# Kernel tuning notes

Measured on AMD Instinct MI355X. Metric: run time of the kernel, lower is better.

The kernel has to match this reference:

```python
import jax, jax.numpy as jnp
import numpy as np

HEADS = 20
SHIFT = 0.6931471805599453  # style_alignment_score_shift = log(2)
KEY_SCALE = 1.0             # style_alignment_score_scale
EPS = 1e-5


def expand_first(feat, scale=1.0):
    # feat: [B, H, S, D]; broadcast style features (batch items 0 and B//2)
    b = feat.shape[0]
    fs = jnp.stack([feat[0], feat[b // 2]])[:, None]           # [2,1,H,S,D]
    fs = jnp.broadcast_to(fs, (2, b // 2) + feat.shape[1:])    # [2,B/2,H,S,D]
    if scale != 1:
        fs = jnp.concatenate([fs[:, :1], scale * fs[:, 1:]], axis=1)
    return fs.reshape(feat.shape)


def concat_first(feat, scale=1.0):
    # concatenate style features along the sequence axis (-2)
    return jnp.concatenate([feat, expand_first(feat, scale=scale)], axis=-2)


def adain(feat):
    # stats over sequence axis (-2); torch .var() is unbiased (ddof=1)
    mean = feat.mean(axis=-2, keepdims=True)
    std = jnp.sqrt(feat.var(axis=-2, keepdims=True, ddof=1) + EPS)
    sm = expand_first(mean)
    ss = expand_first(std)
    return (feat - mean) / std * ss + sm


def setup_inputs() -> dict:
    key = jax.random.key(0)
    ks = jax.random.split(key, 6)
    B, S, C = 4, 1024, 1280
    sc = 1.0 / np.sqrt(C)
    return {
        "hidden_states": jax.random.normal(ks[0], (B, S, C), jnp.float32),
        "Wq": jax.random.normal(ks[1], (C, C), jnp.float32) * sc,
        "Wk": jax.random.normal(ks[2], (C, C), jnp.float32) * sc,
        "Wv": jax.random.normal(ks[3], (C, C), jnp.float32) * sc,
        "Wo": jax.random.normal(ks[4], (C, C), jnp.float32) * sc,
        "bo": jnp.zeros((C,), jnp.float32),
    }


def reference(hidden_states, Wq, Wk, Wv, Wo, bo):
    B, S, C = hidden_states.shape
    H = HEADS
    hd = C // H
    scale = hd ** -0.5

    def to_heads(t):  # [B,S,C] -> [B,H,S,hd]
        return t.reshape(B, S, H, hd).transpose(0, 2, 1, 3)

    q = to_heads(hidden_states @ Wq.T)
    k = to_heads(hidden_states @ Wk.T)
    v = to_heads(hidden_states @ Wv.T)

    q = adain(q)              # adain_queries
    k = adain(k)              # adain_keys
    # adain_values = False

    k = concat_first(k, scale=KEY_SCALE)   # [B,H,2S,hd]
    v = concat_first(v)                    # [B,H,2S,hd]

    # shifted scaled dot-product attention (shift added to shared-key block)
    logits = jnp.einsum('bhqd,bhkd->bhqk', q, k) * scale  # [B,H,S,2S]
    bias = jnp.where(jnp.arange(k.shape[-2]) >= S, jnp.float32(SHIFT), jnp.float32(0.0))
    probs = jax.nn.softmax(logits + bias, axis=-1)
    out = jnp.einsum('bhqk,bhkd->bhqd', probs, v)         # [B,H,S,hd]

    out = out.transpose(0, 2, 1, 3).reshape(B, S, C)
    out = out @ Wo.T + bo
    return out
```

## Files before the change

kernel.cpp:

```cpp
#include <hip/hip_runtime.h>
#include <math.h>


typedef __bf16 bf16x8 __attribute__((ext_vector_type(8)));
typedef __bf16 bf16x2_t __attribute__((ext_vector_type(2)));
typedef float f32x4 __attribute__((ext_vector_type(4)));
typedef unsigned short u16x8 __attribute__((ext_vector_type(8)));

#define BDIM 256

__device__ inline unsigned short f2bf(float f) {
  return __builtin_bit_cast(unsigned short, (__bf16)f);
}
__device__ inline unsigned int pack_bf2(float lo, float hi) {
  bf16x2_t v;
  v[0] = (__bf16)lo;
  v[1] = (__bf16)hi;
  return __builtin_bit_cast(unsigned int, v);
}
__device__ inline float bf2f(unsigned short h) {
  return __uint_as_float(((unsigned int)h) << 16);
}

__device__ inline void gl_lds16(const unsigned short* g, unsigned short* l) {
  __builtin_amdgcn_global_load_lds(
      (const __attribute__((address_space(1))) unsigned int*)g,
      (__attribute__((address_space(3))) unsigned int*)l, 16, 0, 0);
}

__global__ __launch_bounds__(BDIM) void k_convert_all(
    const float* __restrict__ X, const float* __restrict__ Wq,
    const float* __restrict__ Wk, const float* __restrict__ Wv,
    const float* __restrict__ Wo, unsigned short* __restrict__ Xbf,
    unsigned short* __restrict__ Wcat, unsigned short* __restrict__ Wobf) {
  const int idx = blockIdx.x * BDIM + threadIdx.x;
  const float* src;
  unsigned short* dst;
  int off;
  if (idx < 1310720) {
    src = X; dst = Xbf; off = idx;
  } else {
    const int r = idx - 1310720;
    const int which = r / 409600;
    off = r - which * 409600;
    src = (which == 0) ? Wq : (which == 1) ? Wk : (which == 2) ? Wv : Wo;
    dst = (which < 3) ? Wcat + (size_t)which * 1638400 : Wobf;
  }
  const float4 v = ((const float4*)src)[off];
  ushort4 o;
  o.x = f2bf(v.x); o.y = f2bf(v.y); o.z = f2bf(v.z); o.w = f2bf(v.w);
  ((ushort4*)dst)[off] = o;
}

__global__ __launch_bounds__(512, 1) void k_gemm_bf16(
    const unsigned short* __restrict__ A, const unsigned short* __restrict__ B,
    unsigned short* __restrict__ qb, unsigned short* __restrict__ kb,
    unsigned short* __restrict__ vb, int M, int N, int K) {
  __shared__ unsigned short lds[4][2][256 * 32];

  const int bid = blockIdx.x;
  const int swz = (bid & 7) * 30 + (bid >> 3);
  const int mt = swz & 15, nt = swz >> 4;
  const int mBase = mt * 256, nBase = nt * 256;
  const int r3 = nt / 5;
  unsigned short* Cb = (r3 == 0) ? qb : (r3 == 1) ? kb : vb;
  const int nOff = nBase - r3 * 1280;

  const int t = threadIdx.x;
  const int w = t >> 6, lane = t & 63, quad = lane >> 4, l16 = lane & 15;
  const int wrow = w & 1, wcol = w >> 1;
  const int NTILES = K >> 5;

  f32x4 acc[8][4];
#pragma unroll
  for (int i = 0; i < 8; ++i)
#pragma unroll
    for (int j = 0; j < 4; ++j) acc[i][j] = (f32x4){0.f, 0.f, 0.f, 0.f};

  const int srow = t >> 2;
  const int sgl = ((t & 3) ^ ((t >> 3) & 3)) * 8;

  auto stage = [&](int s, int kt) {
#pragma unroll
    for (int j = 0; j < 2; ++j) {
      const int row = j * 128 + srow;
      gl_lds16(A + (size_t)(mBase + row) * K + kt * 32 + sgl,
               &lds[s][0][(j * 512 + t) * 8]);
    }
#pragma unroll
    for (int j = 0; j < 2; ++j) {
      const int row = j * 128 + srow;
      gl_lds16(B + (size_t)(nBase + row) * K + kt * 32 + sgl,
               &lds[s][1][(j * 512 + t) * 8]);
    }
  };

  stage(0, 0);
  stage(1, 1);

  const int arow0 = (wrow * 128 + l16) * 32;
  const int brow0 = (wcol * 64 + l16) * 32;
  const int gsw = (quad ^ ((l16 >> 1) & 3)) * 8;

  for (int kt = 0; kt < NTILES; ++kt) {
    const int s = kt & 3;
    if (kt + 2 < NTILES) {
      stage((kt + 2) & 3, kt + 2);
      asm volatile("s_waitcnt vmcnt(8)" ::: "memory");
    } else if (kt + 1 < NTILES) {
      asm volatile("s_waitcnt vmcnt(4)" ::: "memory");
    } else {
      asm volatile("s_waitcnt vmcnt(0)" ::: "memory");
    }
    __builtin_amdgcn_s_barrier();

    const unsigned short* As = &lds[s][0][0];
    const unsigned short* Bs = &lds[s][1][0];
    bf16x8 af[8], bq[4];
#pragma unroll
    for (int mi = 0; mi < 8; ++mi)
      af[mi] = *(const bf16x8*)(As + arow0 + mi * 512 + gsw);
#pragma unroll
    for (int ni = 0; ni < 4; ++ni)
      bq[ni] = *(const bf16x8*)(Bs + brow0 + ni * 512 + gsw);
    __builtin_amdgcn_s_setprio(1);
#pragma unroll
    for (int mi = 0; mi < 8; ++mi)
#pragma unroll
      for (int ni = 0; ni < 4; ++ni)
        acc[mi][ni] = __builtin_amdgcn_mfma_f32_16x16x32_bf16(
            af[mi], bq[ni], acc[mi][ni], 0, 0, 0);
    __builtin_amdgcn_s_setprio(0);
  }

#pragma unroll
  for (int mi = 0; mi < 8; ++mi)
#pragma unroll
    for (int r = 0; r < 4; ++r) {
      const int row = mBase + wrow * 128 + mi * 16 + quad * 4 + r;
#pragma unroll
      for (int ni = 0; ni < 4; ++ni)
        Cb[(size_t)row * 1280 + nOff + wcol * 64 + ni * 16 + l16] =
            f2bf(acc[mi][ni][r]);
    }
}

__global__ __launch_bounds__(BDIM, 2) void k_gemm_out(
    const unsigned short* __restrict__ A, const unsigned short* __restrict__ B,
    float* __restrict__ Cf, const float* __restrict__ bias, int M, int N,
    int K) {
  __shared__ unsigned short lds[4][2][128 * 32];

  const int bid = blockIdx.x;
  const int swz = (bid & 7) * 40 + (bid >> 3);
  const int mt = swz & 31, nt = swz >> 5;
  const int mBase = mt * 128, nBase = nt * 128;

  const int t = threadIdx.x;
  const int w = t >> 6, lane = t & 63, quad = lane >> 4, l16 = lane & 15;
  const int wrow = w & 1, wcol = w >> 1;
  const int NTILES = K >> 5;

  f32x4 acc[4][4];
#pragma unroll
  for (int i = 0; i < 4; ++i)
#pragma unroll
    for (int j = 0; j < 4; ++j) acc[i][j] = (f32x4){0.f, 0.f, 0.f, 0.f};

  const int srow = t >> 2;
  const int sgl = ((t & 3) ^ ((t >> 3) & 3)) * 8;

  auto stage = [&](int s, int kt) {
#pragma unroll
    for (int j = 0; j < 2; ++j) {
      const int row = j * 64 + srow;
      gl_lds16(A + (size_t)(mBase + row) * K + kt * 32 + sgl,
               &lds[s][0][(j * 256 + t) * 8]);
    }
#pragma unroll
    for (int j = 0; j < 2; ++j) {
      const int row = j * 64 + srow;
      gl_lds16(B + (size_t)(nBase + row) * K + kt * 32 + sgl,
               &lds[s][1][(j * 256 + t) * 8]);
    }
  };

  stage(0, 0);
  stage(1, 1);

  const int arow0 = (wrow * 64 + l16) * 32;
  const int brow0 = (wcol * 64 + l16) * 32;
  const int gsw = (quad ^ ((l16 >> 1) & 3)) * 8;

  for (int kt = 0; kt < NTILES; ++kt) {
    const int s = kt & 3;
    if (kt + 2 < NTILES) {
      stage((kt + 2) & 3, kt + 2);
      asm volatile("s_waitcnt vmcnt(8)" ::: "memory");
    } else if (kt + 1 < NTILES) {
      asm volatile("s_waitcnt vmcnt(4)" ::: "memory");
    } else {
      asm volatile("s_waitcnt vmcnt(0)" ::: "memory");
    }
    __builtin_amdgcn_s_barrier();

    const unsigned short* As = &lds[s][0][0];
    const unsigned short* Bs = &lds[s][1][0];
    bf16x8 af[4], bq[4];
#pragma unroll
    for (int mi = 0; mi < 4; ++mi)
      af[mi] = *(const bf16x8*)(As + arow0 + mi * 512 + gsw);
#pragma unroll
    for (int ni = 0; ni < 4; ++ni)
      bq[ni] = *(const bf16x8*)(Bs + brow0 + ni * 512 + gsw);
    __builtin_amdgcn_s_setprio(1);
#pragma unroll
    for (int mi = 0; mi < 4; ++mi)
#pragma unroll
      for (int ni = 0; ni < 4; ++ni)
        acc[mi][ni] = __builtin_amdgcn_mfma_f32_16x16x32_bf16(
            af[mi], bq[ni], acc[mi][ni], 0, 0, 0);
    __builtin_amdgcn_s_setprio(0);
  }

#pragma unroll
  for (int mi = 0; mi < 4; ++mi)
#pragma unroll
    for (int r = 0; r < 4; ++r) {
      const int row = mBase + wrow * 64 + mi * 16 + quad * 4 + r;
#pragma unroll
      for (int ni = 0; ni < 4; ++ni) {
        const int col = nBase + wcol * 64 + ni * 16 + l16;
        Cf[(size_t)row * N + col] = acc[mi][ni][r] + bias[col];
      }
    }
}

__global__ __launch_bounds__(320) void k_stats1(
    const unsigned short* __restrict__ qb, const unsigned short* __restrict__ kb,
    float* __restrict__ psum, float* __restrict__ psq) {
  const int z = blockIdx.y, which = z >> 2, b = z & 3;
  const unsigned short* src = (which == 0) ? qb : kb;
  const int c = threadIdx.x * 4;
  const size_t base = (size_t)(b * 1024 + blockIdx.x * 32) * 1280 + c;
  float4 s = {0.f, 0.f, 0.f, 0.f}, s2 = {0.f, 0.f, 0.f, 0.f};
#pragma unroll 8
  for (int i = 0; i < 32; ++i) {
    const ushort4 xv = *(const ushort4*)(src + base + (size_t)i * 1280);
    const float x0 = bf2f(xv.x), x1 = bf2f(xv.y), x2 = bf2f(xv.z),
                x3 = bf2f(xv.w);
    s.x += x0; s.y += x1; s.z += x2; s.w += x3;
    s2.x = fmaf(x0, x0, s2.x); s2.y = fmaf(x1, x1, s2.y);
    s2.z = fmaf(x2, x2, s2.z); s2.w = fmaf(x3, x3, s2.w);
  }
  const size_t o = ((size_t)z * 32 + blockIdx.x) * 1280 + c;
  *(float4*)(psum + o) = s;
  *(float4*)(psq + o) = s2;
}

__global__ __launch_bounds__(BDIM) void k_vt_stats2(
    const unsigned short* __restrict__ vb, unsigned short* __restrict__ vt,
    const float* __restrict__ psum, const float* __restrict__ psq,
    float* __restrict__ fst) {
  const int bx = blockIdx.x;
  if (bx >= 1280) {
    const int fb = bx - 1280;
    const int which = fb / 5;
    const int c = (fb % 5) * 256 + threadIdx.x;
    float m[4], sd[4];
#pragma unroll
    for (int b = 0; b < 4; ++b) {
      const int z = which * 4 + b;
      float s = 0.f, s2 = 0.f;
#pragma unroll
      for (int j = 0; j < 32; ++j) {
        s += psum[((size_t)z * 32 + j) * 1280 + c];
        s2 += psq[((size_t)z * 32 + j) * 1280 + c];
      }
      const float mean = s * (1.0f / 1024.0f);
      const float var = (s2 - 1024.0f * mean * mean) * (1.0f / 1023.0f);
      m[b] = mean;
      sd[b] = sqrtf(var + 1e-5f);
    }
    const float S2 = 0.125f * 1.44269504088896341f;
#pragma unroll
    for (int b = 0; b < 4; ++b) {
      const int bs = (b < 2) ? 0 : 2;
      const float g = sd[bs] / sd[b];
      const float o = m[bs] - m[b] * g;
      if (which == 0) {
        fst[(0 * 4 + b) * 1280 + c] = g;
        fst[(1 * 4 + b) * 1280 + c] = o;
      } else {
        fst[(2 * 4 + b) * 1280 + c] = g * S2;
        fst[(3 * 4 + b) * 1280 + c] = o;
      }
    }
    return;
  }
  __shared__ unsigned short tile[64][65];
  const int b = bx / 320;
  const int r2 = bx - b * 320;
  const int c0 = (r2 / 16) * 64;
  const int s0 = (r2 & 15) * 64;
  const int t = threadIdx.x;
  const int r = t >> 2, seg = (t & 3) * 16;
  const size_t goff = ((size_t)(b * 1024 + s0 + r)) * 1280 + c0 + seg;
  const u16x8 va = *(const u16x8*)(vb + goff);
  const u16x8 vv = *(const u16x8*)(vb + goff + 8);
#pragma unroll
  for (int j = 0; j < 8; j++) {
    tile[r][seg + j] = va[j];
    tile[r][seg + 8 + j] = vv[j];
  }
  __syncthreads();
  u16x8 o0, o1;
#pragma unroll
  for (int j = 0; j < 8; j++) {
    o0[j] = tile[seg + j][r];
    o1[j] = tile[seg + 8 + j][r];
  }
  const size_t ooff = ((size_t)(b * 1280 + c0 + r)) * 1024 + s0 + seg;
  *(u16x8*)(vt + ooff) = o0;
  *(u16x8*)(vt + ooff + 8) = o1;
}

__global__ __launch_bounds__(BDIM, 4) void k_attn(
    const unsigned short* __restrict__ qb, const unsigned short* __restrict__ kb,
    const float* __restrict__ fst, const unsigned short* __restrict__ vt,
    unsigned short* __restrict__ Opart, float* __restrict__ Lpart,
    unsigned short* __restrict__ attnb) {
  const int S = 1024;
  const int L = blockIdx.x + 8 * (blockIdx.y + 20 * blockIdx.z);
  const int qt = (L >> 3) & 7;
  const int hz = (L & 7) + ((L >> 6) << 3);
  const int h = hz % 20;
  const int zs = hz / 20;
  int b, ktBeg;
  bool direct;
  if (zs == 0)      { b = 0; ktBeg = 0;  direct = true;  }
  else if (zs == 1) { b = 1; ktBeg = 0;  direct = false; }
  else if (zs == 2) { b = 1; ktBeg = 16; direct = false; }
  else if (zs == 3) { b = 2; ktBeg = 0;  direct = true;  }
  else if (zs == 4) { b = 3; ktBeg = 0;  direct = false; }
  else              { b = 3; ktBeg = 16; direct = false; }
  const int t = threadIdx.x, w = t >> 6, lane = t & 63;
  const int quad = lane >> 4, l16 = lane & 15;
  const int bstyle = (b < 2) ? 0 : 2;
  const int qrow = qt * 128 + w * 32;
  const bool style = (ktBeg >= 16);

  __shared__ unsigned short Ks[2][2][64 * 32];
  __shared__ unsigned short Vs[2][64 * 32];
  __shared__ unsigned short Plds[4][32][64];

  const float S2 = 0.125f * 1.44269504088896341f;

  const int krow = t >> 2;
  const int kseg = ((t & 3) ^ ((t >> 3) & 3)) * 8;
  const int sw = l16 & 14;
  const int qsw = (quad ^ ((l16 >> 1) & 3)) * 8;

  auto stageK = [&](int buf, int kt) {
    const int bs = (kt < 16) ? b : bstyle;
    const int sk = (kt & 15) * 64;
    const unsigned short* kg =
        kb + (size_t)(bs * S + sk + krow) * 1280 + h * 64 + kseg;
    gl_lds16(kg, Ks[buf][0] + t * 8);
    gl_lds16(kg + 32, Ks[buf][1] + t * 8);
  };
  auto stageV = [&](int kt) {
    const int bs = (kt < 16) ? b : bstyle;
    const int sk = (kt & 15) * 64;
    const unsigned short* vg =
        vt + (size_t)(bs * 1280 + h * 64 + krow) * S + sk + kseg;
    gl_lds16(vg, Vs[0] + t * 8);
    gl_lds16(vg + 32, Vs[1] + t * 8);
  };

  stageK(0, ktBeg);

  bf16x8 aq[2][2];
  float biasv[2];
  {
    const int bk = style ? bstyle : b;
    float rq[2] = {0.f, 0.f};
#pragma unroll
    for (int hf = 0; hf < 2; ++hf) {
      const int cc = h * 64 + quad * 8 + hf * 32;
      float gq[8], oq[8], gs[8], ok[8];
      *(float4*)(gq)     = *(const float4*)(fst + (0 * 4 + b) * 1280 + cc);
      *(float4*)(gq + 4) = *(const float4*)(fst + (0 * 4 + b) * 1280 + cc + 4);
      *(float4*)(oq)     = *(const float4*)(fst + (1 * 4 + b) * 1280 + cc);
      *(float4*)(oq + 4) = *(const float4*)(fst + (1 * 4 + b) * 1280 + cc + 4);
      *(float4*)(gs)     = *(const float4*)(fst + (2 * 4 + bk) * 1280 + cc);
      *(float4*)(gs + 4) = *(const float4*)(fst + (2 * 4 + bk) * 1280 + cc + 4);
      *(float4*)(ok)     = *(const float4*)(fst + (3 * 4 + bk) * 1280 + cc);
      *(float4*)(ok + 4) = *(const float4*)(fst + (3 * 4 + bk) * 1280 + cc + 4);
#pragma unroll
      for (int g = 0; g < 2; ++g) {
        const size_t qoff =
            ((size_t)(b * S + qrow + g * 16 + l16)) * 1280 + cc;
        const bf16x8 qv = *(const bf16x8*)(qb + qoff);
        bf16x8 av;
#pragma unroll
        for (int j = 0; j < 8; ++j) {
          const float qn = fmaf((float)qv[j], gq[j], oq[j]);
          rq[g] = fmaf(qn, ok[j], rq[g]);
          av[j] = (__bf16)(qn * gs[j]);
        }
        aq[g][hf] = av;
      }
    }
    const float shift = style ? 1.0f : 0.0f;
#pragma unroll
    for (int g = 0; g < 2; ++g) {
      float r = rq[g] * S2;
      r += __shfl_xor(r, 16, 64);
      r += __shfl_xor(r, 32, 64);
      biasv[g] = shift + r;
    }
  }

  bf16x8 ones;
#pragma unroll
  for (int i = 0; i < 8; ++i) ones[i] = (__bf16)1.0f;

  f32x4 o[2][4], lsum[2];
#pragma unroll
  for (int g = 0; g < 2; ++g) {
    lsum[g] = (f32x4){0.f, 0.f, 0.f, 0.f};
#pragma unroll
    for (int i = 0; i < 4; i++) o[g][i] = (f32x4){0.f, 0.f, 0.f, 0.f};
  }

  for (int i = 0; i < 16; ++i) {
    const int kt = ktBeg + i;
    const int buf = i & 1;
    asm volatile("s_waitcnt vmcnt(0)" ::: "memory");
    __builtin_amdgcn_s_barrier();
    stageV(kt);
    if (i + 1 < 16) stageK(buf ^ 1, kt + 1);

    f32x4 z2[2][4];
#pragma unroll
    for (int nt = 0; nt < 4; ++nt) {
      const bf16x8 bk0 =
          *(const bf16x8*)(Ks[buf][0] + (nt * 16 + l16) * 32 + qsw);
      const bf16x8 bk1 =
          *(const bf16x8*)(Ks[buf][1] + (nt * 16 + l16) * 32 + qsw);
#pragma unroll
      for (int g = 0; g < 2; ++g) {
        f32x4 zz = (f32x4){0.f, 0.f, 0.f, 0.f};
        zz = __builtin_amdgcn_mfma_f32_16x16x32_bf16(bk0, aq[g][0], zz, 0, 0, 0);
        zz = __builtin_amdgcn_mfma_f32_16x16x32_bf16(bk1, aq[g][1], zz, 0, 0, 0);
        z2[g][nt] = zz;
      }
    }

#pragma unroll
    for (int g = 0; g < 2; ++g) {
      const float bg = biasv[g];
#pragma unroll
      for (int nt = 0; nt < 4; ++nt) {
        const float e0 = exp2f(z2[g][nt][0] + bg);
        const float e1 = exp2f(z2[g][nt][1] + bg);
        const float e2 = exp2f(z2[g][nt][2] + bg);
        const float e3 = exp2f(z2[g][nt][3] + bg);
        uint2 pk;
        pk.x = pack_bf2(e0, e1);
        pk.y = pack_bf2(e2, e3);
        const int phys = (nt * 4 + quad) ^ sw;
        *(uint2*)(&Plds[w][g * 16 + l16][phys * 4]) = pk;
      }
    }

    if (i + 1 < 16)
      asm volatile("s_waitcnt vmcnt(2)" ::: "memory");
    else
      asm volatile("s_waitcnt vmcnt(0)" ::: "memory");
    __builtin_amdgcn_s_barrier();

#pragma unroll
    for (int g = 0; g < 2; ++g) {
      const int a0 = (2 * quad) ^ sw;
      const int a1 = (2 * quad + 8) ^ sw;
      const bf16x8 pa0 = *(const bf16x8*)(&Plds[w][g * 16 + l16][a0 * 4]);
      const bf16x8 pa1 = *(const bf16x8*)(&Plds[w][g * 16 + l16][a1 * 4]);
      lsum[g] = __builtin_amdgcn_mfma_f32_16x16x32_bf16(pa0, ones, lsum[g], 0, 0, 0);
      lsum[g] = __builtin_amdgcn_mfma_f32_16x16x32_bf16(pa1, ones, lsum[g], 0, 0, 0);
#pragma unroll
      for (int dt = 0; dt < 4; ++dt) {
        const bf16x8 vb0 =
            *(const bf16x8*)(Vs[0] + (dt * 16 + l16) * 32 + qsw);
        const bf16x8 vb1 =
            *(const bf16x8*)(Vs[1] + (dt * 16 + l16) * 32 + qsw);
        o[g][dt] =
            __builtin_amdgcn_mfma_f32_16x16x32_bf16(pa0, vb0, o[g][dt], 0, 0, 0);
        o[g][dt] =
            __builtin_amdgcn_mfma_f32_16x16x32_bf16(pa1, vb1, o[g][dt], 0, 0, 0);
      }
    }
  }

  if (direct) {
    unsigned short* ab =
        attnb + ((size_t)(b * S + qrow)) * 1280 + h * 64;
#pragma unroll
    for (int g = 0; g < 2; ++g)
#pragma unroll
      for (int r = 0; r < 4; ++r) {
        const float rl = 1.0f / lsum[g][r];
        const int ro = (g * 16 + quad * 4 + r) * 1280;
#pragma unroll
        for (int dt = 0; dt < 4; ++dt)
          ab[ro + dt * 16 + l16] = f2bf(o[g][dt][r] * rl);
      }
  } else {
    const int slice = (zs < 3) ? (zs - 1) : (zs - 2);
    if (l16 == 0) {
#pragma unroll
      for (int g = 0; g < 2; ++g)
#pragma unroll
        for (int r = 0; r < 4; ++r)
          Lpart[((size_t)slice * 20 + h) * 1024 + qrow + g * 16 + quad * 4 +
                r] = lsum[g][r];
    }
    unsigned short* Op = Opart + (size_t)slice * 1310720;
#pragma unroll
    for (int g = 0; g < 2; ++g)
#pragma unroll
      for (int dt = 0; dt < 4; ++dt)
#pragma unroll
        for (int r = 0; r < 4; ++r)
          Op[(size_t)(qrow + g * 16 + quad * 4 + r) * 1280 + h * 64 + dt * 16 +
             l16] = f2bf(o[g][dt][r]);
  }
}

__global__ __launch_bounds__(BDIM) void k_combine(
    const unsigned short* __restrict__ Opart, const float* __restrict__ Lpart,
    unsigned short* __restrict__ attnb) {
  const int idx = blockIdx.x * BDIM + threadIdx.x;
  const int row = idx / 160;
  const int c = (idx - row * 160) * 8;
  const int bb = row >> 10;
  const int q = row & 1023;
  const int h = c >> 6;
  const int s0 = bb * 2;
  float L = 0.f;
  float acc[8] = {0.f, 0.f, 0.f, 0.f, 0.f, 0.f, 0.f, 0.f};
#pragma unroll
  for (int s = 0; s < 2; ++s) {
    const int z = s0 + s;
    L += Lpart[((size_t)z * 20 + h) * 1024 + q];
    const u16x8 v =
        *(const u16x8*)(Opart + (size_t)z * 1310720 + (size_t)q * 1280 + c);
#pragma unroll
    for (int j = 0; j < 8; ++j) acc[j] += bf2f(v[j]);
  }
  const float rl = 1.0f / L;
  const int orow = (bb * 2 + 1) * 1024 + q;
  u16x8 o8;
#pragma unroll
  for (int j = 0; j < 8; ++j) o8[j] = f2bf(acc[j] * rl);
  *(u16x8*)(attnb + (size_t)orow * 1280 + c) = o8;
}

extern "C" void kernel_launch(void* const* d_in, const int* in_sizes, int n_in,
                              void* d_out, int out_size, void* d_ws,
                              size_t ws_size, hipStream_t stream) {
  const float* X = (const float*)d_in[0];
  const float* Wq = (const float*)d_in[1];
  const float* Wk = (const float*)d_in[2];
  const float* Wv = (const float*)d_in[3];
  const float* Wo = (const float*)d_in[4];
  const float* bo = (const float*)d_in[5];
  float* out = (float*)d_out;

  char* ws = (char*)d_ws;
  size_t off = 0;
  auto alloc = [&](size_t bytes) {
    char* p = ws + off;
    off += (bytes + 255) & ~(size_t)255;
    return p;
  };
  unsigned short* Wcat = (unsigned short*)alloc(3840ull * 1280 * 2);
  unsigned short* Xbf = (unsigned short*)alloc(4096ull * 1280 * 2);
  unsigned short* qbb = (unsigned short*)alloc(4096ull * 1280 * 2);
  unsigned short* kbb = (unsigned short*)alloc(4096ull * 1280 * 2);
  unsigned short* vbb = (unsigned short*)alloc(4096ull * 1280 * 2);
  unsigned short* Wobf = (unsigned short*)alloc(1280ull * 1280 * 2);
  float* fstats = (float*)alloc(4ull * 4 * 1280 * 4);
  unsigned short* qnb = (unsigned short*)alloc(4096ull * 1280 * 2);
  unsigned short* knb = (unsigned short*)alloc(4096ull * 1280 * 2);
  unsigned short* vtb = (unsigned short*)alloc(4096ull * 1280 * 2);
  unsigned short* attnb = (unsigned short*)alloc(4096ull * 1280 * 2);
  (void)qnb;
  (void)knb;

  unsigned short* Opart = Xbf;
  float* Lpart = (float*)Wcat;
  float* psum = (float*)attnb;
  float* psq = (float*)(attnb + 4096ull * 1280 / 2);

  k_convert_all<<<11520, BDIM, 0, stream>>>(X, Wq, Wk, Wv, Wo, Xbf, Wcat, Wobf);
  k_gemm_bf16<<<240, 512, 0, stream>>>(Xbf, Wcat, qbb, kbb, vbb, 4096, 3840,
                                       1280);
  k_stats1<<<dim3(32, 8), 320, 0, stream>>>(qbb, kbb, psum, psq);
  k_vt_stats2<<<1290, BDIM, 0, stream>>>(vbb, vtb, psum, psq, fstats);
  k_attn<<<dim3(8, 20, 6), BDIM, 0, stream>>>(qbb, kbb, fstats, vtb, Opart,
                                              Lpart, attnb);
  k_combine<<<1280, BDIM, 0, stream>>>(Opart, Lpart, attnb);
  k_gemm_out<<<320, BDIM, 0, stream>>>(attnb, Wobf, out, bo, 4096, 1280, 1280);
}
```

Measured before the change: 242.5 us.

## Double-buffer V tiles and drop mid-iteration barrier in attention loop

```diff
diff --git a/kernel.cpp b/kernel.cpp
--- a/kernel.cpp
+++ b/kernel.cpp
@@ -351,8 +351,8 @@
   const bool style = (ktBeg >= 16);
 
   __shared__ unsigned short Ks[2][2][64 * 32];
-  __shared__ unsigned short Vs[2][64 * 32];
-  __shared__ unsigned short Plds[4][32][64];
+  __shared__ unsigned short Vs[2][2][64 * 32];
+  __shared__ unsigned short Plds[4][16][64];
 
   const float S2 = 0.125f * 1.44269504088896341f;
 
@@ -369,16 +369,17 @@
     gl_lds16(kg, Ks[buf][0] + t * 8);
     gl_lds16(kg + 32, Ks[buf][1] + t * 8);
   };
-  auto stageV = [&](int kt) {
+  auto stageV = [&](int buf, int kt) {
     const int bs = (kt < 16) ? b : bstyle;
     const int sk = (kt & 15) * 64;
     const unsigned short* vg =
         vt + (size_t)(bs * 1280 + h * 64 + krow) * S + sk + kseg;
-    gl_lds16(vg, Vs[0] + t * 8);
-    gl_lds16(vg + 32, Vs[1] + t * 8);
+    gl_lds16(vg, Vs[buf][0] + t * 8);
+    gl_lds16(vg + 32, Vs[buf][1] + t * 8);
   };
 
   stageK(0, ktBeg);
+  stageV(0, ktBeg);
 
   bf16x8 aq[2][2];
   float biasv[2];
@@ -439,8 +440,10 @@
     const int buf = i & 1;
     asm volatile("s_waitcnt vmcnt(0)" ::: "memory");
     __builtin_amdgcn_s_barrier();
-    stageV(kt);
-    if (i + 1 < 16) stageK(buf ^ 1, kt + 1);
+    if (i + 1 < 16) {
+      stageK(buf ^ 1, kt + 1);
+      stageV(buf ^ 1, kt + 1);
+    }
 
     f32x4 z2[2][4];
 #pragma unroll
@@ -471,30 +474,20 @@
         pk.x = pack_bf2(e0, e1);
         pk.y = pack_bf2(e2, e3);
         const int phys = (nt * 4 + quad) ^ sw;
-        *(uint2*)(&Plds[w][g * 16 + l16][phys * 4]) = pk;
-      }
-    }
-
-    if (i + 1 < 16)
-      asm volatile("s_waitcnt vmcnt(2)" ::: "memory");
-    else
-      asm volatile("s_waitcnt vmcnt(0)" ::: "memory");
-    __builtin_amdgcn_s_barrier();
-
-#pragma unroll
-    for (int g = 0; g < 2; ++g) {
+        *(uint2*)(&Plds[w][l16][phys * 4]) = pk;
+      }
       const int a0 = (2 * quad) ^ sw;
       const int a1 = (2 * quad + 8) ^ sw;
-      const bf16x8 pa0 = *(const bf16x8*)(&Plds[w][g * 16 + l16][a0 * 4]);
-      const bf16x8 pa1 = *(const bf16x8*)(&Plds[w][g * 16 + l16][a1 * 4]);
+      const bf16x8 pa0 = *(const bf16x8*)(&Plds[w][l16][a0 * 4]);
+      const bf16x8 pa1 = *(const bf16x8*)(&Plds[w][l16][a1 * 4]);
       lsum[g] = __builtin_amdgcn_mfma_f32_16x16x32_bf16(pa0, ones, lsum[g], 0, 0, 0);
       lsum[g] = __builtin_amdgcn_mfma_f32_16x16x32_bf16(pa1, ones, lsum[g], 0, 0, 0);
 #pragma unroll
       for (int dt = 0; dt < 4; ++dt) {
         const bf16x8 vb0 =
-            *(const bf16x8*)(Vs[0] + (dt * 16 + l16) * 32 + qsw);
+            *(const bf16x8*)(Vs[buf][0] + (dt * 16 + l16) * 32 + qsw);
         const bf16x8 vb1 =
-            *(const bf16x8*)(Vs[1] + (dt * 16 + l16) * 32 + qsw);
+            *(const bf16x8*)(Vs[buf][1] + (dt * 16 + l16) * 32 + qsw);
         o[g][dt] =
             __builtin_amdgcn_mfma_f32_16x16x32_bf16(pa0, vb0, o[g][dt], 0, 0, 0);
         o[g][dt] =
```

New measurement: 242.0 us. Within noise of the previous version (-0.2%).
